# Optimization experiments

Measured on AMD Instinct MI355X. Metric: run time of the kernel, lower is better.

Reference implementation:

```python
import jax, jax.numpy as jnp
import numpy as np

# torch.finfo(torch.float16).tiny — the fill value the original uses for masked logits
FP16_TINY = 6.103515625e-05


def setup_inputs() -> dict:
    key = jax.random.key(0)
    k1, k2, k3 = jax.random.split(key, 3)
    B, V = 128, 128000
    logits = jax.random.normal(k1, (B, V), dtype=jnp.float32)
    k = jax.random.randint(k2, (B,), 1, 64)  # top-k in [1, 64)
    p = jax.random.uniform(k3, (B,), dtype=jnp.float32)  # top-p in [0, 1)
    return {"logits": logits, "k": k, "p": p, "no_top_k": 0, "no_top_p": 0}


def _apply_top_k_top_p(logits, no_top_k, k, no_top_p, p):
    if no_top_k and no_top_p:
        return logits
    # Ascending sort along vocab (matches torch descending=False)
    logits_idx = jnp.argsort(logits, axis=-1)                       # [B, V]
    logits_sort = jnp.take_along_axis(logits, logits_idx, axis=-1)  # [B, V]
    V = logits_sort.shape[-1]
    if not no_top_k:
        # threshold = value at position V - k (k-th largest); mask everything below it
        thresh_idx = (V - k).astype(jnp.int32)[:, None]             # [B, 1]
        thresh = jnp.take_along_axis(logits_sort, thresh_idx, axis=-1)
        logits_sort = jnp.where(logits_sort < thresh, FP16_TINY, logits_sort)
    if not no_top_p:
        probs_sort = jax.nn.softmax(logits_sort, axis=-1)
        probs_sum = jnp.cumsum(probs_sort, axis=-1)
        top_p_mask = probs_sum <= (1.0 - p)[:, None]
        top_p_mask = top_p_mask.at[:, -1].set(False)  # always keep the max logit
        logits_sort = jnp.where(top_p_mask, FP16_TINY, logits_sort)
    # Scatter masked values back to original positions (inverse permutation gather)
    inv_idx = jnp.argsort(logits_idx, axis=-1)
    return jnp.take_along_axis(logits_sort, inv_idx, axis=-1)


def reference(logits, k, p, no_top_k, no_top_p):
    masked = _apply_top_k_top_p(logits, no_top_k, k, no_top_p, p)
    return jax.nn.softmax(masked.astype(jnp.float32), axis=-1)
```

## Files before the change

kernel.cpp:

```cpp
#include <hip/hip_runtime.h>
#include <math.h>


#define VOCAB 128000
#define NROWS 128
#define BPR 25
#define F4T 5
#define CHUNK (256 * F4T * 4)
#define BCAP 64
#define CTHRESH 3.0f
#define TINYV 6.103515625e-05
#define SORTN 512
#define KMAX 128
#define FBR 5
#define FCHUNK (VOCAB / FBR)
#define FF4 (FCHUNK / 4 / 256)

typedef unsigned long long u64;
typedef unsigned int u32;
typedef float f4 __attribute__((ext_vector_type(4)));

__global__ void __launch_bounds__(256) filter_k(const float* __restrict__ logits,
                                                int* __restrict__ segcnt,
                                                u64* __restrict__ cand) {
    __shared__ u64 sbuf[BCAP];
    __shared__ int scnt;
    const int row = blockIdx.y;
    const int bx  = blockIdx.x;
    const int tid = threadIdx.x;
    if (tid == 0) scnt = 0;
    __syncthreads();

    const int base = bx * CHUNK;
    const f4* src = (const f4*)(logits + (size_t)row * VOCAB + base);
    f4 v[F4T];
#pragma unroll
    for (int j = 0; j < F4T; ++j)
        v[j] = __builtin_nontemporal_load(&src[j * 256 + tid]);
#pragma unroll
    for (int j = 0; j < F4T; ++j) {
#pragma unroll
        for (int e = 0; e < 4; ++e) {
            float x = v[j][e];
            if (x > CTHRESH) {
                int p = atomicAdd(&scnt, 1);
                u32 idx = (u32)(base + j * 1024 + tid * 4 + e);
                if (p < BCAP)
                    sbuf[p] = ((u64)__float_as_uint(x) << 32) | idx;
            }
        }
    }
    __syncthreads();
    int n = scnt < BCAP ? scnt : BCAP;
    const int seg = row * BPR + bx;
    if (tid == 0) segcnt[seg] = n;
    if (tid < n) cand[(size_t)seg * BCAP + tid] = sbuf[tid];
}

__global__ void __launch_bounds__(256) fused_k(const u64* __restrict__ cand,
                                               const int* __restrict__ segcnt,
                                               const int* __restrict__ kk,
                                               const float* __restrict__ pp,
                                               const int* __restrict__ no_top_p,
                                               float* __restrict__ out) {
    __shared__ u64 s[SORTN];
    __shared__ double ed[KMAX];
    __shared__ int cnts[BPR], pfx[BPR + 1];
    __shared__ int snf;
    __shared__ double sZp;
    __shared__ float stiny;
    const int row = blockIdx.y;
    const int bx  = blockIdx.x;
    const int tid = threadIdx.x;

    if (tid < BPR) cnts[tid] = segcnt[row * BPR + tid];
    __syncthreads();
    if (tid == 0) {
        int acc = 0;
        for (int i = 0; i < BPR; ++i) { pfx[i] = acc; acc += cnts[i]; }
        pfx[BPR] = acc;
    }
    __syncthreads();
    for (int sl = tid; sl < BPR * BCAP; sl += 256) {
        int sg = sl >> 6, j = sl & (BCAP - 1);
        if (j < cnts[sg]) {
            int d = pfx[sg] + j;
            if (d < SORTN) s[d] = cand[(size_t)(row * BPR + sg) * BCAP + j];
        }
    }
    __syncthreads();
    int c = pfx[BPR];
    if (c > SORTN) c = SORTN;

    u64 myk[2]; int myr[2];
#pragma unroll
    for (int t = 0; t < 2; ++t) {
        int i = tid + t * 256;
        myr[t] = -1;
        if (i < c) {
            u64 ki = s[i];
            int r = 0;
            for (int j = 0; j < c; ++j) r += (s[j] > ki);
            myk[t] = ki; myr[t] = r;
        }
    }
    __syncthreads();
#pragma unroll
    for (int t = 0; t < 2; ++t)
        if (myr[t] >= 0) s[myr[t]] = myk[t];
    __syncthreads();

    const double M = (double)__uint_as_float((u32)(s[0] >> 32));
    if (tid < KMAX)
        ed[tid] = (tid < c)
                    ? exp((double)__uint_as_float((u32)(s[tid] >> 32)) - M)
                    : 0.0;
    __syncthreads();

    if (tid == 0) {
        int kq = kk[row];
        if (kq < 1) kq = 1;
        if (kq > c) kq = c;
        const float Tk = __uint_as_float((u32)(s[kq - 1] >> 32));
        int n_keep = kq;
        while (n_keep < c && n_keep < KMAX &&
               __uint_as_float((u32)(s[n_keep] >> 32)) >= Tk) ++n_keep;

        const double q = exp((double)TINYV - M);
        const double bulk = (double)(VOCAB - n_keep) * q;
        double sum_top = 0.0;
        for (int i = n_keep - 1; i >= 0; --i) sum_top += ed[i];
        const double Z = bulk + sum_top;

        int jstar = 0;
        if (no_top_p[0] == 0) {
            const double tZ = (1.0 - (double)pp[row]) * Z;
            double csum = bulk;
            jstar = n_keep - 1;
            for (int l = 0; l < n_keep; ++l) {
                csum += ed[n_keep - 1 - l];
                if (csum > tZ) { jstar = l; break; }
            }
        }
        const int n_final = n_keep - jstar;

        double Zp = (double)(VOCAB - n_final) * q;
        for (int i = 0; i < n_final; ++i) Zp += ed[i];

        snf   = n_final;
        sZp   = Zp;
        stiny = (float)(q / Zp);
    }
    __syncthreads();

    const int base = bx * FCHUNK;
    int   pidx = -1;
    float pval = 0.f;
    if (tid < snf) {
        int idx = (int)(u32)s[tid];
        if (idx >= base && idx < base + FCHUNK) {
            pidx = idx;
            pval = (float)(ed[tid] / sZp);
        }
    }

    const float tp = stiny;
    f4 o4; o4[0] = tp; o4[1] = tp; o4[2] = tp; o4[3] = tp;
    f4* dst = (f4*)(out + (size_t)row * VOCAB + base);
#pragma unroll
    for (int i = 0; i < FF4; ++i)
        __builtin_nontemporal_store(o4, &dst[i * 256 + tid]);

    __threadfence_block();
    __syncthreads();
    if (pidx >= 0)
        out[(size_t)row * VOCAB + pidx] = pval;
}

extern "C" void kernel_launch(void* const* d_in, const int* in_sizes, int n_in,
                              void* d_out, int out_size, void* d_ws, size_t ws_size,
                              hipStream_t stream) {
    const float* logits = (const float*)d_in[0];
    const int*   kk     = (const int*)d_in[1];
    const float* pp     = (const float*)d_in[2];
    const int*   ntp    = (const int*)d_in[4];
    float* out = (float*)d_out;

    char* ws = (char*)d_ws;
    int* segcnt = (int*)ws;
    u64* cand   = (u64*)(ws + 16384);

    hipLaunchKernelGGL(filter_k, dim3(BPR, NROWS), dim3(256), 0, stream,
                       logits, segcnt, cand);
    hipLaunchKernelGGL(fused_k, dim3(FBR, NROWS), dim3(256), 0, stream,
                       cand, segcnt, kk, pp, ntp, out);
}
```

Measured before the change: 128.7 us.

## Fuse filter and sampler kernels with intra-row spin-wait flag synchronization

Merges the candidate-filter kernel and the top-k/top-p output kernel into one launch with 5 blocks per row. Each block writes its candidates and an encoded flag, then spin-waits on its sibling blocks' flags before sorting and writing output. This removes a kernel launch and the inter-kernel gap, but cuts filter parallelism from 25 to 5 blocks per row. It also relies on all sibling blocks being co-resident; the flag encoding is not reset between calls, so stale flags from a previous run could be read as valid.

```diff
diff --git a/kernel.cpp b/kernel.cpp
--- a/kernel.cpp
+++ b/kernel.cpp
@@ -4,92 +4,109 @@
 
 #define VOCAB 128000
 #define NROWS 128
-#define BPR 25
-#define F4T 5
-#define CHUNK (256 * F4T * 4)
-#define BCAP 64
+#define FBR 5
+#define FCHUNK (VOCAB / FBR)
+#define FF4 (FCHUNK / 4 / 256)
+#define GCAP 128
 #define CTHRESH 3.0f
 #define TINYV 6.103515625e-05
 #define SORTN 512
 #define KMAX 128
-#define FBR 5
-#define FCHUNK (VOCAB / FBR)
-#define FF4 (FCHUNK / 4 / 256)
+#define MAGIC16 0xA5C3u
 
 typedef unsigned long long u64;
 typedef unsigned int u32;
 typedef float f4 __attribute__((ext_vector_type(4)));
 
-__global__ void __launch_bounds__(256) filter_k(const float* __restrict__ logits,
-                                                int* __restrict__ segcnt,
-                                                u64* __restrict__ cand) {
-    __shared__ u64 sbuf[BCAP];
+__device__ __forceinline__ u32 enc_flag(int n) {
+    return ((((u32)n) ^ MAGIC16) << 16) | (u32)n;
+}
+
+__global__ void __launch_bounds__(256, 3)
+sampler_k(const float* __restrict__ logits,
+          const int* __restrict__ kk,
+          const float* __restrict__ pp,
+          const int* __restrict__ no_top_p,
+          float* __restrict__ out,
+          u32* __restrict__ flag,
+          u64* __restrict__ cand) {
+    __shared__ u64 sbuf[GCAP];
     __shared__ int scnt;
+    __shared__ u64 s[SORTN];
+    __shared__ double ed[KMAX];
+    __shared__ int cnts[FBR], pfx[FBR + 1];
+    __shared__ int snf;
+    __shared__ double sZp;
+    __shared__ float stiny;
+
     const int row = blockIdx.y;
     const int bx  = blockIdx.x;
     const int tid = threadIdx.x;
+    const int seg = row * FBR + bx;
     if (tid == 0) scnt = 0;
     __syncthreads();
 
-    const int base = bx * CHUNK;
-    const f4* src = (const f4*)(logits + (size_t)row * VOCAB + base);
-    f4 v[F4T];
-#pragma unroll
-    for (int j = 0; j < F4T; ++j)
-        v[j] = __builtin_nontemporal_load(&src[j * 256 + tid]);
-#pragma unroll
-    for (int j = 0; j < F4T; ++j) {
-#pragma unroll
-        for (int e = 0; e < 4; ++e) {
-            float x = v[j][e];
-            if (x > CTHRESH) {
-                int p = atomicAdd(&scnt, 1);
-                u32 idx = (u32)(base + j * 1024 + tid * 4 + e);
-                if (p < BCAP)
-                    sbuf[p] = ((u64)__float_as_uint(x) << 32) | idx;
+    const size_t rbase = (size_t)row * VOCAB;
+    const int base = bx * FCHUNK;
+    const f4* src = (const f4*)(logits + rbase + base);
+#pragma unroll 1
+    for (int g = 0; g < 5; ++g) {
+        f4 v[5];
+#pragma unroll
+        for (int j = 0; j < 5; ++j)
+            v[j] = src[(g * 5 + j) * 256 + tid];
+#pragma unroll
+        for (int j = 0; j < 5; ++j) {
+#pragma unroll
+            for (int e = 0; e < 4; ++e) {
+                float x = v[j][e];
+                if (x > CTHRESH) {
+                    int p = atomicAdd(&scnt, 1);
+                    u32 idx = (u32)(base + (g * 5 + j) * 1024 + tid * 4 + e);
+                    if (p < GCAP)
+                        sbuf[p] = ((u64)__float_as_uint(x) << 32) | idx;
+                }
             }
         }
     }
     __syncthreads();
-    int n = scnt < BCAP ? scnt : BCAP;
-    const int seg = row * BPR + bx;
-    if (tid == 0) segcnt[seg] = n;
-    if (tid < n) cand[(size_t)seg * BCAP + tid] = sbuf[tid];
-}
-
-__global__ void __launch_bounds__(256) fused_k(const u64* __restrict__ cand,
-                                               const int* __restrict__ segcnt,
-                                               const int* __restrict__ kk,
-                                               const float* __restrict__ pp,
-                                               const int* __restrict__ no_top_p,
-                                               float* __restrict__ out) {
-    __shared__ u64 s[SORTN];
-    __shared__ double ed[KMAX];
-    __shared__ int cnts[BPR], pfx[BPR + 1];
-    __shared__ int snf;
-    __shared__ double sZp;
-    __shared__ float stiny;
-    const int row = blockIdx.y;
-    const int bx  = blockIdx.x;
-    const int tid = threadIdx.x;
-
-    if (tid < BPR) cnts[tid] = segcnt[row * BPR + tid];
-    __syncthreads();
+    int n = scnt < GCAP ? scnt : GCAP;
+    if (tid < n) cand[(size_t)seg * GCAP + tid] = sbuf[tid];
+    __syncthreads();
+    if (tid == 0)
+        __hip_atomic_store(&flag[seg], enc_flag(n),
+                           __ATOMIC_RELEASE, __HIP_MEMORY_SCOPE_AGENT);
+
+    if (tid < FBR) {
+        u32 f;
+        int tries = 0, cnt = 0;
+        for (;;) {
+            f = __hip_atomic_load(&flag[row * FBR + tid],
+                                  __ATOMIC_RELAXED, __HIP_MEMORY_SCOPE_AGENT);
+            u32 lo = f & 0xFFFFu, hi = f >> 16;
+            if (((hi ^ lo) == MAGIC16) && lo <= GCAP) { cnt = (int)lo; break; }
+            if (++tries > (1 << 27)) { cnt = 0; break; }
+        }
+        cnts[tid] = cnt;
+    }
+    __syncthreads();
+    __threadfence();
+
     if (tid == 0) {
         int acc = 0;
-        for (int i = 0; i < BPR; ++i) { pfx[i] = acc; acc += cnts[i]; }
-        pfx[BPR] = acc;
-    }
-    __syncthreads();
-    for (int sl = tid; sl < BPR * BCAP; sl += 256) {
-        int sg = sl >> 6, j = sl & (BCAP - 1);
+        for (int i = 0; i < FBR; ++i) { pfx[i] = acc; acc += cnts[i]; }
+        pfx[FBR] = acc;
+    }
+    __syncthreads();
+    for (int sl = tid; sl < FBR * GCAP; sl += 256) {
+        int sg = sl >> 7, j = sl & (GCAP - 1);
         if (j < cnts[sg]) {
             int d = pfx[sg] + j;
-            if (d < SORTN) s[d] = cand[(size_t)(row * BPR + sg) * BCAP + j];
-        }
-    }
-    __syncthreads();
-    int c = pfx[BPR];
+            if (d < SORTN) s[d] = cand[(size_t)(row * FBR + sg) * GCAP + j];
+        }
+    }
+    __syncthreads();
+    int c = pfx[FBR];
     if (c > SORTN) c = SORTN;
 
     u64 myk[2]; int myr[2];
@@ -153,7 +170,6 @@
     }
     __syncthreads();
 
-    const int base = bx * FCHUNK;
     int   pidx = -1;
     float pval = 0.f;
     if (tid < snf) {
@@ -166,7 +182,7 @@
 
     const float tp = stiny;
     f4 o4; o4[0] = tp; o4[1] = tp; o4[2] = tp; o4[3] = tp;
-    f4* dst = (f4*)(out + (size_t)row * VOCAB + base);
+    f4* dst = (f4*)(out + rbase + base);
 #pragma unroll
     for (int i = 0; i < FF4; ++i)
         __builtin_nontemporal_store(o4, &dst[i * 256 + tid]);
@@ -174,7 +190,7 @@
     __threadfence_block();
     __syncthreads();
     if (pidx >= 0)
-        out[(size_t)row * VOCAB + pidx] = pval;
+        out[rbase + pidx] = pval;
 }
 
 extern "C" void kernel_launch(void* const* d_in, const int* in_sizes, int n_in,
@@ -187,11 +203,9 @@
     float* out = (float*)d_out;
 
     char* ws = (char*)d_ws;
-    int* segcnt = (int*)ws;
-    u64* cand   = (u64*)(ws + 16384);
-
-    hipLaunchKernelGGL(filter_k, dim3(BPR, NROWS), dim3(256), 0, stream,
-                       logits, segcnt, cand);
-    hipLaunchKernelGGL(fused_k, dim3(FBR, NROWS), dim3(256), 0, stream,
-                       cand, segcnt, kk, pp, ntp, out);
+    u32* flag = (u32*)ws;
+    u64* cand = (u64*)(ws + 16384);
+
+    hipLaunchKernelGGL(sampler_k, dim3(FBR, NROWS), dim3(256), 0, stream,
+                       logits, kk, pp, ntp, out, flag, cand);
 }
```

New measurement: 189.2 us. 1.47x slower.
